# Kernel tuning notes

Measured on AMD Instinct MI355X. Metric: run time of the kernel, lower is better.

The kernel has to match this reference:

```python
import jax, jax.numpy as jnp
import numpy as np
from math import comb

N_VARS = 6
DEGREE = 4
NUM_TERMS = 768
D1 = DEGREE + 1          # coeffs per variable row (input)
D2 = 2 * DEGREE + 1      # coeffs per variable row after squaring


def _bern_mul_weights(d):
    # Bernstein-basis product: c_k = sum_i C(d,i)C(d,k-i)/C(2d,k) a_i b_{k-i}
    W = np.zeros((d + 1, d + 1, 2 * d + 1), dtype=np.float32)
    for i in range(d + 1):
        for j in range(d + 1):
            W[i, j, i + j] = comb(d, i) * comb(d, j) / comb(2 * d, i + j)
    return W

_W_NP = _bern_mul_weights(DEGREE)          # (D1, D1, D2) product weights
_E_NP = _W_NP.sum(axis=1)                  # (D1, D2) degree elevation d -> 2d (multiply by ones poly)


def ibf_minmax(P):
    """Interval bounds of an implicit-Bernstein-form poly P: (T, V, D1).
    Per term: interval of each var row (Bernstein coeff min/max bound the poly on [0,1]),
    interval product across vars, then interval sum across terms."""
    lo = P.min(-1)  # (T, V)
    hi = P.max(-1)
    T = P.shape[0]
    ones = jnp.ones((T,), P.dtype)

    def step(carry, x):
        clo, chi = carry
        xlo, xhi = x
        cand = jnp.stack([clo * xlo, clo * xhi, chi * xlo, chi * xhi])
        return (cand.min(0), cand.max(0)), None

    (tlo, thi), _ = jax.lax.scan(step, (ones, ones), (lo.T, hi.T))  # scan over V vars
    return tlo.sum(), thi.sum()


def relu_coeffs_under(l, u):
    # quadratic lower relaxation of ReLU on [l,u]: q(x) = (x^2 - l x)/(u - l)
    den = jnp.where(u - l > 0, u - l, jnp.ones_like(u))
    quad = jnp.stack([1.0 / den, -l / den, jnp.zeros_like(l)])
    lin = jnp.array([0.0, 1.0, 0.0], dtype=quad.dtype)
    zero = jnp.zeros(3, dtype=quad.dtype)
    return jnp.where(l >= 0, lin, jnp.where(u <= 0, zero, quad))


def relu_coeffs_over(l, u):
    # quadratic upper relaxation: q(x) = u (x - l)^2 / (u - l)^2
    den = jnp.where(u - l > 0, u - l, jnp.ones_like(u))
    d2 = den * den
    quad = jnp.stack([u / d2, -2.0 * u * l / d2, u * l * l / d2])
    lin = jnp.array([0.0, 1.0, 0.0], dtype=quad.dtype)
    zero = jnp.zeros(3, dtype=quad.dtype)
    return jnp.where(l >= 0, lin, jnp.where(u <= 0, zero, quad))


def quad_of_poly(P, coeffs):
    """Compose quadratic a x^2 + b x + c with IBF poly P (T, V, D1).
    Returns IBF poly with T^2 + T + 1 terms, per-var degree 2*DEGREE."""
    a, b, c = coeffs[0], coeffs[1], coeffs[2]
    W = jnp.asarray(_W_NP)
    E = jnp.asarray(_E_NP)
    T, V, _ = P.shape
    # P^2: all pairwise term products; per-var Bernstein row product
    sq = jnp.einsum('tvi,svj,ijk->tsvk', P, P, W).reshape(T * T, V, D2)
    sq = sq.at[:, 0, :].multiply(a)          # scale by a on first var row
    # b * P: elevate each row from degree d to 2d, scale by b
    lin = jnp.einsum('tvi,ik->tvk', P, E)
    lin = lin.at[:, 0, :].multiply(b)
    # constant term c: all-ones rows, first row scaled by c
    const = jnp.ones((1, V, D2), P.dtype).at[0, 0, :].multiply(c)
    out = jnp.concatenate([sq, lin, const], axis=0)  # (T^2+T+1, V, D2)
    return out.reshape((T * T + T + 1) * V, D2)


def setup_inputs() -> dict:
    key = jax.random.key(0)
    k1, k2 = jax.random.split(key)
    input_under = jax.random.normal(k1, (NUM_TERMS * N_VARS, D1), dtype=jnp.float32)
    input_over = jax.random.normal(k2, (NUM_TERMS * N_VARS, D1), dtype=jnp.float32)
    return {"input_under": input_under, "input_over": input_over}


def reference(input_under, input_over):
    Pu = input_under.reshape(input_under.shape[0] // N_VARS, N_VARS, D1)
    Po = input_over.reshape(input_over.shape[0] // N_VARS, N_VARS, D1)
    l = ibf_minmax(Pu)[0]
    u = ibf_minmax(Po)[1]
    # torch.tensor([l, u]) detaches in the original -> stop_gradient for faithfulness
    l = jax.lax.stop_gradient(l)
    u = jax.lax.stop_gradient(u)
    cu = relu_coeffs_under(l, u)
    co = relu_coeffs_over(l, u)
    relu_node_under = quad_of_poly(Pu, cu)
    relu_node_over = quad_of_poly(Po, co)
    return relu_node_under, relu_node_over
```

## Files before the change

kernel.cpp:

```cpp
#include <hip/hip_runtime.h>

#define T_TERMS 768
#define NV 6
#define D1 5
#define D2 9
#define T2 (T_TERMS * T_TERMS)
#define PTOT (T2 + T_TERMS + 1)
#define NROWS ((unsigned int)PTOT * NV)
#define NOUT (NROWS * (unsigned int)D2)

typedef float f4 __attribute__((ext_vector_type(4)));
typedef float f4u __attribute__((ext_vector_type(4), aligned(4)));
typedef float f2 __attribute__((ext_vector_type(2)));

__global__ void bounds_kernel(const float* __restrict__ Pu,
                              const float* __restrict__ Po,
                              float* __restrict__ ws) {
    const float* __restrict__ P = blockIdx.x ? Po : Pu;
    int t = threadIdx.x;
    float acc = 0.f;
    if (t < T_TERMS) {
        f2 r[15];
        const f2* p2 = (const f2*)(P + t * (NV * D1));
        #pragma unroll
        for (int i = 0; i < 15; ++i) r[i] = p2[i];
        const float* rf = (const float*)r;
        float clo = 1.f, chi = 1.f;
        #pragma unroll
        for (int v = 0; v < NV; ++v) {
            float lo = rf[v * 5 + 0], hi = lo;
            #pragma unroll
            for (int i = 1; i < 5; ++i) {
                float x = rf[v * 5 + i];
                lo = fminf(lo, x); hi = fmaxf(hi, x);
            }
            float a = clo * lo, b = clo * hi, c = chi * lo, d = chi * hi;
            clo = fminf(fminf(a, b), fminf(c, d));
            chi = fmaxf(fmaxf(a, b), fmaxf(c, d));
        }
        acc = blockIdx.x ? chi : clo;
    }
    __shared__ float sred[12];
    for (int off = 32; off; off >>= 1) acc += __shfl_down(acc, off);
    int wave = threadIdx.x >> 6;
    if ((threadIdx.x & 63) == 0) sred[wave] = acc;
    __syncthreads();
    if (threadIdx.x == 0) {
        float s = 0.f;
        #pragma unroll
        for (int w = 0; w < 12; ++w) s += sred[w];
        ws[blockIdx.x] = s;
    }
}

__global__ void coef_kernel(float* __restrict__ ws) {
    float l = ws[0], u = ws[1];
    float den = (u - l > 0.f) ? (u - l) : 1.f;
    float au, bu, cu, ao, bo, co;
    if (l >= 0.f) {
        au = 0.f; bu = 1.f; cu = 0.f;
        ao = 0.f; bo = 1.f; co = 0.f;
    } else if (u <= 0.f) {
        au = bu = cu = 0.f;
        ao = bo = co = 0.f;
    } else {
        au = 1.f / den; bu = -l / den; cu = 0.f;
        float d2 = den * den;
        ao = u / d2; bo = -2.f * u * l / d2; co = u * l * l / d2;
    }
    float* coef = ws + 2;
    coef[0] = au; coef[1] = bu; coef[2] = cu;
    coef[3] = ao; coef[4] = bo; coef[5] = co;
}

__global__ __launch_bounds__(256) void expand_kernel(
        const float* __restrict__ Pu,
        const float* __restrict__ Po,
        const float* __restrict__ coef,
        float* __restrict__ out) {
    __shared__ float lds[256 * D2];
    static constexpr float Wt[5][5] = {
        {1.0f,        4.0f/8.0f,   6.0f/28.0f,  4.0f/56.0f,  1.0f/70.0f},
        {4.0f/8.0f,   16.0f/28.0f, 24.0f/56.0f, 16.0f/70.0f, 4.0f/56.0f},
        {6.0f/28.0f,  24.0f/56.0f, 36.0f/70.0f, 24.0f/56.0f, 6.0f/28.0f},
        {4.0f/56.0f,  16.0f/70.0f, 24.0f/56.0f, 16.0f/28.0f, 4.0f/8.0f},
        {1.0f/70.0f,  4.0f/56.0f,  6.0f/28.0f,  4.0f/8.0f,   1.0f}
    };

    const unsigned tid = threadIdx.x;
    const unsigned bid = blockIdx.x;
    const unsigned ten = blockIdx.y;
    const float* __restrict__ P = ten ? Po : Pu;
    const float* __restrict__ c3 = coef + ten * 3;

    const unsigned rr = bid * 256u + tid;
    const unsigned nvalid = min(256u, NROWS - bid * 256u);

    float c[9] = {0.f,0.f,0.f,0.f,0.f,0.f,0.f,0.f,0.f};
    if (rr < NROWS) {
        unsigned p = rr / 6u;
        unsigned v = rr - p * 6u;
        f4 a4; float a1;
        f4 b4; float b1;
        float scale = 1.f;
        if (p < (unsigned)T2) {
            unsigned t = p / (unsigned)T_TERMS;
            unsigned s = p - t * (unsigned)T_TERMS;
            const float* A = P + (t * NV + v) * D1;
            const float* B = P + (s * NV + v) * D1;
            a4 = *(const f4u*)A;  a1 = A[4];
            b4 = *(const f4u*)B;  b1 = B[4];
            if (v == 0u) scale = c3[0];
        } else if (p < (unsigned)(T2 + T_TERMS)) {
            unsigned t = p - (unsigned)T2;
            const float* A = P + (t * NV + v) * D1;
            a4 = *(const f4u*)A;  a1 = A[4];
            b4 = (f4){1.f,1.f,1.f,1.f};  b1 = 1.f;
            if (v == 0u) scale = c3[1];
        } else {
            a4 = (f4){1.f,1.f,1.f,1.f};  a1 = 1.f;
            b4 = (f4){1.f,1.f,1.f,1.f};  b1 = 1.f;
            if (v == 0u) scale = c3[2];
        }
        float a[5] = {a4.x * scale, a4.y * scale, a4.z * scale, a4.w * scale, a1 * scale};
        float b[5] = {b4.x, b4.y, b4.z, b4.w, b1};
        #pragma unroll
        for (int i = 0; i < 5; ++i)
            #pragma unroll
            for (int j = 0; j < 5; ++j)
                c[i + j] = fmaf(Wt[i][j] * a[i], b[j], c[i + j]);
    }
    #pragma unroll
    for (int k = 0; k < 9; ++k) lds[tid * 9u + k] = c[k];
    __syncthreads();

    float* __restrict__ o = out + (size_t)ten * NOUT + (size_t)bid * (256u * D2);
    if (nvalid == 256u) {
        const f4* l4 = (const f4*)lds;
        f4* o4 = (f4*)o;
        o4[tid]         = l4[tid];
        o4[tid + 256u]  = l4[tid + 256u];
        if (tid < 64u)
            o4[tid + 512u] = l4[tid + 512u];
    } else {
        const unsigned nd = nvalid * 9u;
        for (unsigned x = tid; x < nd; x += 256u)
            o[x] = lds[x];
    }
}

extern "C" void kernel_launch(void* const* d_in, const int* in_sizes, int n_in,
                              void* d_out, int out_size, void* d_ws, size_t ws_size,
                              hipStream_t stream) {
    const float* Pu = (const float*)d_in[0];
    const float* Po = (const float*)d_in[1];
    float* ws = (float*)d_ws;
    float* out = (float*)d_out;

    bounds_kernel<<<2, 768, 0, stream>>>(Pu, Po, ws);
    coef_kernel<<<1, 1, 0, stream>>>(ws);

    unsigned int blocks_x = (NROWS + 255u) / 256u;
    dim3 grid(blocks_x, 2, 1);
    expand_kernel<<<grid, 256, 0, stream>>>(Pu, Po, ws + 2, out);
}
```

Measured before the change: 253.3 us.

## Fuse bounds and coef kernels and make expand a persistent tiled kernel

The bounds and coefficient kernels are merged into one single-block kernel that reduces both tensors and computes the ReLU relaxation coefficients, removing one launch. The expand kernel becomes a fixed 2048-block persistent grid where each block walks a contiguous range of 256-row tiles across both tensors, instead of one block per tile. Stores for the over tensor, whose base is only 8-byte aligned, are realigned to 16-byte vector stores by repacking from LDS. This adds extra barriers per tile and serialises the bounds reduction onto one block.

Measured after the change: 259.2 us. +2.3%, slower.

```diff
diff --git a/kernel.cpp b/kernel.cpp
--- a/kernel.cpp
+++ b/kernel.cpp
@@ -8,20 +8,26 @@
 #define PTOT (T2 + T_TERMS + 1)
 #define NROWS ((unsigned int)PTOT * NV)
 #define NOUT (NROWS * (unsigned int)D2)
+#define ROWS_PER_TILE 256u
+#define TILE_DW (ROWS_PER_TILE * D2)
+#define NTILES ((NROWS + ROWS_PER_TILE - 1u) / ROWS_PER_TILE)
+#define TOTAL_TILES (NTILES * 2u)
+#define NBLOCKS 2048u
+#define CHUNK_Q (TOTAL_TILES / NBLOCKS)
+#define CHUNK_R (TOTAL_TILES % NBLOCKS)
 
 typedef float f4 __attribute__((ext_vector_type(4)));
 typedef float f4u __attribute__((ext_vector_type(4), aligned(4)));
 typedef float f2 __attribute__((ext_vector_type(2)));
 
-__global__ void bounds_kernel(const float* __restrict__ Pu,
-                              const float* __restrict__ Po,
-                              float* __restrict__ ws) {
-    const float* __restrict__ P = blockIdx.x ? Po : Pu;
+__global__ void bounds_coef_kernel(const float* __restrict__ Pu,
+                                   const float* __restrict__ Po,
+                                   float* __restrict__ ws) {
     int t = threadIdx.x;
-    float acc = 0.f;
+    float tlo = 0.f, thi = 0.f;
     if (t < T_TERMS) {
         f2 r[15];
-        const f2* p2 = (const f2*)(P + t * (NV * D1));
+        const f2* p2 = (const f2*)(Pu + t * (NV * D1));
         #pragma unroll
         for (int i = 0; i < 15; ++i) r[i] = p2[i];
         const float* rf = (const float*)r;
@@ -38,39 +44,53 @@
             clo = fminf(fminf(a, b), fminf(c, d));
             chi = fmaxf(fmaxf(a, b), fmaxf(c, d));
         }
-        acc = blockIdx.x ? chi : clo;
-    }
-    __shared__ float sred[12];
-    for (int off = 32; off; off >>= 1) acc += __shfl_down(acc, off);
+        tlo = clo;
+        const f2* q2 = (const f2*)(Po + t * (NV * D1));
+        #pragma unroll
+        for (int i = 0; i < 15; ++i) r[i] = q2[i];
+        clo = 1.f; chi = 1.f;
+        #pragma unroll
+        for (int v = 0; v < NV; ++v) {
+            float lo = rf[v * 5 + 0], hi = lo;
+            #pragma unroll
+            for (int i = 1; i < 5; ++i) {
+                float x = rf[v * 5 + i];
+                lo = fminf(lo, x); hi = fmaxf(hi, x);
+            }
+            float a = clo * lo, b = clo * hi, c = chi * lo, d = chi * hi;
+            clo = fminf(fminf(a, b), fminf(c, d));
+            chi = fmaxf(fmaxf(a, b), fmaxf(c, d));
+        }
+        thi = chi;
+    }
+    __shared__ float slo[12], shi[12];
+    for (int off = 32; off; off >>= 1) {
+        tlo += __shfl_down(tlo, off);
+        thi += __shfl_down(thi, off);
+    }
     int wave = threadIdx.x >> 6;
-    if ((threadIdx.x & 63) == 0) sred[wave] = acc;
+    if ((threadIdx.x & 63) == 0) { slo[wave] = tlo; shi[wave] = thi; }
     __syncthreads();
     if (threadIdx.x == 0) {
-        float s = 0.f;
-        #pragma unroll
-        for (int w = 0; w < 12; ++w) s += sred[w];
-        ws[blockIdx.x] = s;
-    }
-}
-
-__global__ void coef_kernel(float* __restrict__ ws) {
-    float l = ws[0], u = ws[1];
-    float den = (u - l > 0.f) ? (u - l) : 1.f;
-    float au, bu, cu, ao, bo, co;
-    if (l >= 0.f) {
-        au = 0.f; bu = 1.f; cu = 0.f;
-        ao = 0.f; bo = 1.f; co = 0.f;
-    } else if (u <= 0.f) {
-        au = bu = cu = 0.f;
-        ao = bo = co = 0.f;
-    } else {
-        au = 1.f / den; bu = -l / den; cu = 0.f;
-        float d2 = den * den;
-        ao = u / d2; bo = -2.f * u * l / d2; co = u * l * l / d2;
-    }
-    float* coef = ws + 2;
-    coef[0] = au; coef[1] = bu; coef[2] = cu;
-    coef[3] = ao; coef[4] = bo; coef[5] = co;
+        float l = 0.f, u = 0.f;
+        #pragma unroll
+        for (int w = 0; w < 12; ++w) { l += slo[w]; u += shi[w]; }
+        float den = (u - l > 0.f) ? (u - l) : 1.f;
+        float au, bu, cu, ao, bo, co;
+        if (l >= 0.f) {
+            au = 0.f; bu = 1.f; cu = 0.f;
+            ao = 0.f; bo = 1.f; co = 0.f;
+        } else if (u <= 0.f) {
+            au = bu = cu = 0.f;
+            ao = bo = co = 0.f;
+        } else {
+            au = 1.f / den; bu = -l / den; cu = 0.f;
+            float d2 = den * den;
+            ao = u / d2; bo = -2.f * u * l / d2; co = u * l * l / d2;
+        }
+        ws[0] = au; ws[1] = bu; ws[2] = cu;
+        ws[3] = ao; ws[4] = bo; ws[5] = co;
+    }
 }
 
 __global__ __launch_bounds__(256) void expand_kernel(
@@ -78,7 +98,7 @@
         const float* __restrict__ Po,
         const float* __restrict__ coef,
         float* __restrict__ out) {
-    __shared__ float lds[256 * D2];
+    __shared__ float lds[TILE_DW];
     static constexpr float Wt[5][5] = {
         {1.0f,        4.0f/8.0f,   6.0f/28.0f,  4.0f/56.0f,  1.0f/70.0f},
         {4.0f/8.0f,   16.0f/28.0f, 24.0f/56.0f, 16.0f/70.0f, 4.0f/56.0f},
@@ -88,64 +108,95 @@
     };
 
     const unsigned tid = threadIdx.x;
-    const unsigned bid = blockIdx.x;
-    const unsigned ten = blockIdx.y;
-    const float* __restrict__ P = ten ? Po : Pu;
-    const float* __restrict__ c3 = coef + ten * 3;
-
-    const unsigned rr = bid * 256u + tid;
-    const unsigned nvalid = min(256u, NROWS - bid * 256u);
-
-    float c[9] = {0.f,0.f,0.f,0.f,0.f,0.f,0.f,0.f,0.f};
-    if (rr < NROWS) {
-        unsigned p = rr / 6u;
-        unsigned v = rr - p * 6u;
-        f4 a4; float a1;
-        f4 b4; float b1;
-        float scale = 1.f;
-        if (p < (unsigned)T2) {
-            unsigned t = p / (unsigned)T_TERMS;
-            unsigned s = p - t * (unsigned)T_TERMS;
-            const float* A = P + (t * NV + v) * D1;
-            const float* B = P + (s * NV + v) * D1;
-            a4 = *(const f4u*)A;  a1 = A[4];
-            b4 = *(const f4u*)B;  b1 = B[4];
-            if (v == 0u) scale = c3[0];
-        } else if (p < (unsigned)(T2 + T_TERMS)) {
-            unsigned t = p - (unsigned)T2;
-            const float* A = P + (t * NV + v) * D1;
-            a4 = *(const f4u*)A;  a1 = A[4];
-            b4 = (f4){1.f,1.f,1.f,1.f};  b1 = 1.f;
-            if (v == 0u) scale = c3[1];
+    const unsigned b = blockIdx.x;
+    const unsigned gstart = b * CHUNK_Q + (b < CHUNK_R ? b : CHUNK_R);
+    const unsigned gcnt = CHUNK_Q + (b < CHUNK_R ? 1u : 0u);
+
+    for (unsigned gi = 0; gi < gcnt; ++gi) {
+        const unsigned g = gstart + gi;
+        const unsigned ten = (g >= NTILES) ? 1u : 0u;
+        const unsigned tile = ten ? g - NTILES : g;
+        const float* __restrict__ P = ten ? Po : Pu;
+        const float* __restrict__ c3 = coef + ten * 3u;
+
+        const unsigned rr = tile * ROWS_PER_TILE + tid;
+        const unsigned nvalid = min(ROWS_PER_TILE, NROWS - tile * ROWS_PER_TILE);
+
+        float c[9] = {0.f,0.f,0.f,0.f,0.f,0.f,0.f,0.f,0.f};
+        if (rr < NROWS) {
+            unsigned p = rr / 6u;
+            unsigned v = rr - p * 6u;
+            f4 a4; float a1;
+            f4 b4; float b1;
+            float scale = 1.f;
+            if (p < (unsigned)T2) {
+                unsigned t = p / (unsigned)T_TERMS;
+                unsigned s = p - t * (unsigned)T_TERMS;
+                const float* A = P + (t * NV + v) * D1;
+                const float* B = P + (s * NV + v) * D1;
+                a4 = *(const f4u*)A;  a1 = A[4];
+                b4 = *(const f4u*)B;  b1 = B[4];
+                if (v == 0u) scale = c3[0];
+            } else if (p < (unsigned)(T2 + T_TERMS)) {
+                unsigned t = p - (unsigned)T2;
+                const float* A = P + (t * NV + v) * D1;
+                a4 = *(const f4u*)A;  a1 = A[4];
+                b4 = (f4){1.f,1.f,1.f,1.f};  b1 = 1.f;
+                if (v == 0u) scale = c3[1];
+            } else {
+                a4 = (f4){1.f,1.f,1.f,1.f};  a1 = 1.f;
+                b4 = (f4){1.f,1.f,1.f,1.f};  b1 = 1.f;
+                if (v == 0u) scale = c3[2];
+            }
+            float a[5] = {a4.x * scale, a4.y * scale, a4.z * scale, a4.w * scale, a1 * scale};
+            float bb[5] = {b4.x, b4.y, b4.z, b4.w, b1};
+            #pragma unroll
+            for (int i = 0; i < 5; ++i)
+                #pragma unroll
+                for (int j = 0; j < 5; ++j)
+                    c[i + j] = fmaf(Wt[i][j] * a[i], bb[j], c[i + j]);
+        }
+
+        __syncthreads();
+        #pragma unroll
+        for (int k = 0; k < 9; ++k) lds[tid * 9u + k] = c[k];
+        __syncthreads();
+
+        float* __restrict__ ob = out + (size_t)ten * NOUT + (size_t)tile * TILE_DW;
+        if (nvalid == ROWS_PER_TILE) {
+            if (ten == 0u) {
+                const f4* l4 = (const f4*)lds;
+                f4* o4 = (f4*)ob;
+                o4[tid]         = l4[tid];
+                o4[tid + 256u]  = l4[tid + 256u];
+                if (tid < 64u) o4[tid + 512u] = l4[tid + 512u];
+            } else {
+                if (tid < 2u) ob[tid] = lds[tid];
+                if (tid >= 2u && tid < 4u) ob[2300u + tid] = lds[2300u + tid];
+                const f2* l2 = (const f2*)lds;
+                {
+                    unsigned q = tid;
+                    f2 x = l2[1u + 2u * q], y = l2[2u + 2u * q];
+                    f4 vv; vv.x = x.x; vv.y = x.y; vv.z = y.x; vv.w = y.y;
+                    *(f4*)(ob + 2u + 4u * q) = vv;
+                }
+                {
+                    unsigned q = tid + 256u;
+                    f2 x = l2[1u + 2u * q], y = l2[2u + 2u * q];
+                    f4 vv; vv.x = x.x; vv.y = x.y; vv.z = y.x; vv.w = y.y;
+                    *(f4*)(ob + 2u + 4u * q) = vv;
+                }
+                if (tid < 63u) {
+                    unsigned q = tid + 512u;
+                    f2 x = l2[1u + 2u * q], y = l2[2u + 2u * q];
+                    f4 vv; vv.x = x.x; vv.y = x.y; vv.z = y.x; vv.w = y.y;
+                    *(f4*)(ob + 2u + 4u * q) = vv;
+                }
+            }
         } else {
-            a4 = (f4){1.f,1.f,1.f,1.f};  a1 = 1.f;
-            b4 = (f4){1.f,1.f,1.f,1.f};  b1 = 1.f;
-            if (v == 0u) scale = c3[2];
-        }
-        float a[5] = {a4.x * scale, a4.y * scale, a4.z * scale, a4.w * scale, a1 * scale};
-        float b[5] = {b4.x, b4.y, b4.z, b4.w, b1};
-        #pragma unroll
-        for (int i = 0; i < 5; ++i)
-            #pragma unroll
-            for (int j = 0; j < 5; ++j)
-                c[i + j] = fmaf(Wt[i][j] * a[i], b[j], c[i + j]);
-    }
-    #pragma unroll
-    for (int k = 0; k < 9; ++k) lds[tid * 9u + k] = c[k];
-    __syncthreads();
-
-    float* __restrict__ o = out + (size_t)ten * NOUT + (size_t)bid * (256u * D2);
-    if (nvalid == 256u) {
-        const f4* l4 = (const f4*)lds;
-        f4* o4 = (f4*)o;
-        o4[tid]         = l4[tid];
-        o4[tid + 256u]  = l4[tid + 256u];
-        if (tid < 64u)
-            o4[tid + 512u] = l4[tid + 512u];
-    } else {
-        const unsigned nd = nvalid * 9u;
-        for (unsigned x = tid; x < nd; x += 256u)
-            o[x] = lds[x];
+            const unsigned nd = nvalid * 9u;
+            for (unsigned x = tid; x < nd; x += 256u) ob[x] = lds[x];
+        }
     }
 }
 
@@ -157,10 +208,7 @@
     float* ws = (float*)d_ws;
     float* out = (float*)d_out;
 
-    bounds_kernel<<<2, 768, 0, stream>>>(Pu, Po, ws);
-    coef_kernel<<<1, 1, 0, stream>>>(ws);
-
-    unsigned int blocks_x = (NROWS + 255u) / 256u;
-    dim3 grid(blocks_x, 2, 1);
-    expand_kernel<<<grid, 256, 0, stream>>>(Pu, Po, ws + 2, out);
+    bounds_coef_kernel<<<1, 768, 0, stream>>>(Pu, Po, ws);
+
+    expand_kernel<<<NBLOCKS, 256, 0, stream>>>(Pu, Po, ws, out);
 }
```
